# Optimization experiments

Measured on AMD Instinct MI355X. Metric: run time of the kernel, lower is better.

## Reference

```python
import jax, jax.numpy as jnp
import numpy as np

SR = 44100
PRE_EMPH = 0.97
FRAME_LEN = int(0.02 * SR)      # 882
FRAME_HOP = FRAME_LEN // 2      # 441
N_FFT = 2048
EPS = 1e-10


def setup_inputs() -> dict:
    key = jax.random.key(0)
    k1, k2 = jax.random.split(key)
    waveform = jax.random.normal(k1, (16, 441000), dtype=jnp.float32)
    # librosa mel filterbank is a fixed nonnegative (n_mels, n_fft//2+1) matrix;
    # a random surrogate keeps the math (dense matmul) identical.
    mel_filters = jax.random.uniform(k2, (60, N_FFT // 2 + 1), dtype=jnp.float32)
    return {"waveform": waveform, "mel_filters": mel_filters}


def _mfdwc(waveform, mel_filters):
    dt = waveform.dtype
    # pre-emphasis: y[0]=x[0], y[t]=x[t]-0.97*x[t-1]
    emph = jnp.concatenate(
        [waveform[:, :1], waveform[:, 1:] - PRE_EMPH * waveform[:, :-1]], axis=1)
    L = emph.shape[1]
    n_frames = 1 + (L - FRAME_LEN) // FRAME_HOP  # static
    idx = jnp.arange(n_frames)[:, None] * FRAME_HOP + jnp.arange(FRAME_LEN)[None, :]
    frames = emph[:, idx]                                   # (B, T, 882)
    window = jnp.asarray(np.hamming(FRAME_LEN), dtype=dt)   # (882,)
    windowed = frames * window
    spec = jnp.fft.rfft(windowed, n=N_FFT, axis=-1)         # (B, T, 1025) complex
    power = jnp.real(spec) ** 2 + jnp.imag(spec) ** 2       # |FFT|^2
    mel = jnp.einsum('mf,btf->btm', mel_filters, power)     # (B, T, 60)
    logmel = jnp.log(mel + EPS)
    # 1-level Haar DWT along mel axis (pywt convention, even length):
    # cA = (x_even + x_odd)/sqrt(2), cD = (x_even - x_odd)/sqrt(2)
    sq2 = jnp.sqrt(jnp.asarray(2.0, dt))
    x_even, x_odd = logmel[..., 0::2], logmel[..., 1::2]
    cA = (x_even + x_odd) / sq2                             # (B, T, 30)
    cD = (x_even - x_odd) / sq2                             # (B, T, 30)
    # delta (window=3, edge-padded): d[t] = a[clamp(t+1)] - a[clamp(t-1)]
    fwd = jnp.concatenate([cA[:, 1:], cA[:, -1:]], axis=1)
    bwd = jnp.concatenate([cA[:, :1], cA[:, :-1]], axis=1)
    delta = fwd - bwd
    feats = jnp.concatenate([cA, delta, cD], axis=-1)       # (B, T, 90)
    mean = jnp.mean(feats, axis=1)
    std = jnp.std(feats, axis=1, ddof=1)                    # torch.std unbiased
    return jnp.concatenate([mean, std], axis=1)             # (B, 180)


def reference(waveform, mel_filters):
    return _mfdwc(waveform, mel_filters)
```

## Files before the change

kernel.cpp:

```cpp
#include <hip/hip_runtime.h>
#include <hip/hip_bf16.h>
#include <math.h>

#define FRAME_LEN 882
#define FRAME_HOP 441
#define NFFT 2048
#define NFRAMES 999
#define NBATCH 16
#define NMEL 60
#define WAVE_LEN 441000
#define PRE_EMPH 0.97f
#define EPS 1e-10f
#define NROWS (NBATCH * NFRAMES)
#define KPAD 1056
#define NKC 33
#define PANEL_ELEMS (NKC * 512)
#define PI_F 3.14159265358979323846f

#define PADI(i) ((i) + ((i) >> 4))

__device__ __forceinline__ int frag_off(int m, int k) {
  return ((k >> 5) * 512) | (((k >> 3) & 3) * 128) | (m * 8) | (k & 7);
}

typedef float vf2 __attribute__((ext_vector_type(2)));
__device__ __forceinline__ vf2 mkv(float x, float y){ vf2 r; r.x = x; r.y = y; return r; }
__device__ __forceinline__ vf2 cmul(vf2 a, vf2 b){ return a.xx * b + mkv(-a.y, a.y) * b.yx; }
__device__ __forceinline__ vf2 rotni(vf2 z){ return mkv(z.y, -z.x); }

__device__ __forceinline__ void dif_group8(vf2* x, vf2 t1) {
  const vf2 C41 = mkv(0.7071067812f, -0.7071067812f);
  vf2 w0 = t1, w1 = cmul(t1, C41), w2 = rotni(w0), w3 = rotni(w1);
  vf2 u, v;
  u=x[0]; v=x[4]; x[0]=u+v; x[4]=cmul(u-v, w0);
  u=x[1]; v=x[5]; x[1]=u+v; x[5]=cmul(u-v, w1);
  u=x[2]; v=x[6]; x[2]=u+v; x[6]=cmul(u-v, w2);
  u=x[3]; v=x[7]; x[3]=u+v; x[7]=cmul(u-v, w3);
  vf2 t2 = cmul(t1, t1), t2r = rotni(t2);
  u=x[0]; v=x[2]; x[0]=u+v; x[2]=cmul(u-v, t2);
  u=x[1]; v=x[3]; x[1]=u+v; x[3]=cmul(u-v, t2r);
  u=x[4]; v=x[6]; x[4]=u+v; x[6]=cmul(u-v, t2);
  u=x[5]; v=x[7]; x[5]=u+v; x[7]=cmul(u-v, t2r);
  vf2 t4 = cmul(t2, t2);
  u=x[0]; v=x[1]; x[0]=u+v; x[1]=cmul(u-v, t4);
  u=x[2]; v=x[3]; x[2]=u+v; x[3]=cmul(u-v, t4);
  u=x[4]; v=x[5]; x[4]=u+v; x[5]=cmul(u-v, t4);
  u=x[6]; v=x[7]; x[6]=u+v; x[7]=cmul(u-v, t4);
}

__device__ __forceinline__ void dif_radix4(vf2* x) {
  vf2 y0 = x[0] + x[2];
  vf2 y2 = x[0] - x[2];
  vf2 y1 = x[1] + x[3];
  vf2 y3 = rotni(x[1] - x[3]);
  x[0] = y0 + y1; x[1] = y0 - y1;
  x[2] = y2 + y3; x[3] = y2 - y3;
}

__global__ __launch_bounds__(256) void fft_pow_kernel(
    const float* __restrict__ wav, __hip_bfloat16* __restrict__ powrF)
{
  __shared__ vf2 lds[NFFT + (NFFT >> 4)];
  const int t  = threadIdx.x;
  const int t0 = 2 * blockIdx.x, t1f = t0 + 1;
  const bool has1 = (t1f < NFRAMES);
  const int b = blockIdx.y;
  const float* w = wav + (size_t)b * WAVE_LEN;
  const int s0 = t0 * FRAME_HOP;
  int s1 = t1f * FRAME_HOP;
  if (s1 > WAVE_LEN - FRAME_LEN) s1 = WAVE_LEN - FRAME_LEN;

  vf2 x[8];
  {
    float sB, cB, sD, cD;
    __sincosf(6.283185307179586f * (float)t / 881.0f, &sB, &cB);
    __sincosf(6.283185307179586f * 256.0f / 881.0f, &sD, &cD);
    vf2 cur  = mkv(cB, sB);
    vf2 step = mkv(cD, sD);
#pragma unroll
    for (int k = 0; k < 8; ++k) {
      int i = k * 256 + t;
      float v1 = 0.f, v2 = 0.f;
      if (i < FRAME_LEN) {
        float win = 0.54f - 0.46f * cur.x;
        int s = s0 + i;
        float e1 = (s > 0) ? (w[s] - PRE_EMPH * w[s - 1]) : w[s];
        v1 = e1 * win;
        int ss = s1 + i;
        v2 = (w[ss] - PRE_EMPH * w[ss - 1]) * win;
      }
      x[k] = mkv(v1, v2);
      cur = cmul(cur, step);
    }
  }

  {
    float sA, cA;
    __sincosf(-PI_F * (float)t / 1024.0f, &sA, &cA);
    dif_group8(x, mkv(cA, sA));
  }
#pragma unroll
  for (int k = 0; k < 8; ++k) lds[PADI(k * 256 + t)] = x[k];
  __syncthreads();

  {
    const int q = t >> 5, r = t & 31;
#pragma unroll
    for (int k = 0; k < 8; ++k) x[k] = lds[PADI(q * 256 + k * 32 + r)];
    float sA, cA;
    __sincosf(-PI_F * (float)r / 128.0f, &sA, &cA);
    dif_group8(x, mkv(cA, sA));
    __syncthreads();
#pragma unroll
    for (int k = 0; k < 8; ++k) lds[PADI(q * 256 + k * 32 + r)] = x[k];
  }
  __syncthreads();

  {
    const int q = t >> 2, r = t & 3;
#pragma unroll
    for (int k = 0; k < 8; ++k) x[k] = lds[PADI(q * 32 + k * 4 + r)];
    float tc = (r == 0) ? 1.0f : (r == 1) ? 0.980785280f : (r == 2) ? 0.923879533f : 0.831469612f;
    float ts = (r == 0) ? 0.0f : (r == 1) ? -0.195090322f : (r == 2) ? -0.382683432f : -0.555570233f;
    dif_group8(x, mkv(tc, ts));
    __syncthreads();
#pragma unroll
    for (int k = 0; k < 8; ++k) lds[PADI(q * 32 + k * 4 + r)] = x[k];
  }
  __syncthreads();

  {
    vf2 xa[4], xb[4];
#pragma unroll
    for (int j = 0; j < 4; ++j) {
      xa[j] = lds[PADI(4 * t + j)];
      xb[j] = lds[PADI(4 * (t + 256) + j)];
    }
    dif_radix4(xa);
    dif_radix4(xb);
    __syncthreads();
#pragma unroll
    for (int j = 0; j < 4; ++j) {
      lds[PADI(4 * t + j)] = xa[j];
      lds[PADI(4 * (t + 256) + j)] = xb[j];
    }
  }
  __syncthreads();

  const int r0g = b * NFRAMES + t0;
  const int r1g = r0g + 1;
  __hip_bfloat16* q0 = powrF + (size_t)(r0g >> 4) * PANEL_ELEMS;
  const int m0 = r0g & 15;
  __hip_bfloat16* q1 = powrF + (size_t)(r1g >> 4) * PANEL_ELEMS;
  const int m1 = r1g & 15;
#pragma unroll
  for (int c = 0; c < 4; ++c) {
    int f = t + 256 * c;
    int j1 = (int)(__brev((unsigned)f) >> 21);
    int j2 = (int)(__brev((unsigned)((NFFT - f) & (NFFT - 1))) >> 21);
    vf2 z = lds[PADI(j1)];
    vf2 y = lds[PADI(j2)];
    float f1r = z.x + y.x, f1i = z.y - y.y;
    float f2r = z.y + y.y, f2i = y.x - z.x;
    float pw1 = 0.25f * (f1r * f1r + f1i * f1i);
    float pw2 = 0.25f * (f2r * f2r + f2i * f2i);
    q0[frag_off(m0, f)] = __float2bfloat16(pw1);
    if (has1) q1[frag_off(m1, f)] = __float2bfloat16(pw2);
  }
  if (t == 0) {
    vf2 z = lds[PADI(1)];
    q0[frag_off(m0, 1024)] = __float2bfloat16(z.x * z.x);
    if (has1) q1[frag_off(m1, 1024)] = __float2bfloat16(z.y * z.y);
  }
  if (t < KPAD - 1025) {
    int f = 1025 + t;
    q0[frag_off(m0, f)] = __float2bfloat16(0.f);
    if (has1) q1[frag_off(m1, f)] = __float2bfloat16(0.f);
  }
}

__global__ __launch_bounds__(256) void filtconv_kernel(
    const float* __restrict__ filt, __hip_bfloat16* __restrict__ filtbF)
{
  const int mm = blockIdx.x;
  __hip_bfloat16* qp = filtbF + (size_t)(mm >> 4) * PANEL_ELEMS;
  const int m = mm & 15;
  for (int k = threadIdx.x; k < KPAD; k += 256) {
    float v = (mm < NMEL && k < 1025) ? filt[mm * 1025 + k] : 0.f;
    qp[frag_off(m, k)] = __float2bfloat16(v);
  }
}

typedef __attribute__((ext_vector_type(8))) short short8x;
typedef __attribute__((ext_vector_type(4))) float float4x;

__global__ __launch_bounds__(256) void melgemm_kernel(
    const __hip_bfloat16* __restrict__ powrF,
    const __hip_bfloat16* __restrict__ filtbF,
    float* __restrict__ logmelT)
{
  const int wave = threadIdx.x >> 6, lane = threadIdx.x & 63;
  const int p = blockIdx.x;
  const __hip_bfloat16* pA = powrF + (size_t)p * PANEL_ELEMS + lane * 8;
  const __hip_bfloat16* pB = filtbF + (size_t)wave * PANEL_ELEMS + lane * 8;

  float4x acc0 = {0.f, 0.f, 0.f, 0.f};
  float4x acc1 = {0.f, 0.f, 0.f, 0.f};
#pragma unroll 4
  for (int kc = 0; kc < 16; ++kc) {
    short8x a0 = *(const short8x*)(pA + kc * 512);
    short8x b0 = *(const short8x*)(pB + kc * 512);
    short8x a1 = *(const short8x*)(pA + (kc + 16) * 512);
    short8x b1 = *(const short8x*)(pB + (kc + 16) * 512);
    acc0 = __builtin_amdgcn_mfma_f32_16x16x32_bf16(a0, b0, acc0, 0, 0, 0);
    acc1 = __builtin_amdgcn_mfma_f32_16x16x32_bf16(a1, b1, acc1, 0, 0, 0);
  }
  {
    short8x a = *(const short8x*)(pA + 32 * 512);
    short8x bf = *(const short8x*)(pB + 32 * 512);
    acc0 = __builtin_amdgcn_mfma_f32_16x16x32_bf16(a, bf, acc0, 0, 0, 0);
  }

  const int mel = wave * 16 + (lane & 15);
  const int rsub = (lane >> 4) * 4;
  if (mel < NMEL) {
#pragma unroll
    for (int reg = 0; reg < 4; ++reg) {
      int row = p * 16 + rsub + reg;
      float vv = acc0[reg] + acc1[reg];
      logmelT[(size_t)mel * NROWS + row] = __logf(vv + EPS);
    }
  }
}

__global__ __launch_bounds__(256) void stats_kernel(
    const float* __restrict__ lmT, float* __restrict__ out)
{
  __shared__ float red[4];
  const int j   = blockIdx.x;
  const int b   = blockIdx.y;
  const int tid = threadIdx.x;
  const int base = b * NFRAMES;
  const float inv_sq2 = 0.7071067811865475f;
  const bool v3 = (tid < NFRAMES - 768);

  float f0, f1, f2, f3;
  if (j < 30) {
    const float* e = lmT + (size_t)(2 * j) * NROWS + base;
    const float* o = lmT + (size_t)(2 * j + 1) * NROWS + base;
    f0 = (e[tid]       + o[tid])       * inv_sq2;
    f1 = (e[tid + 256] + o[tid + 256]) * inv_sq2;
    f2 = (e[tid + 512] + o[tid + 512]) * inv_sq2;
    f3 = v3 ? (e[tid + 768] + o[tid + 768]) * inv_sq2 : 0.f;
  } else if (j < 60) {
    const int m = j - 30;
    const float* e = lmT + (size_t)(2 * m) * NROWS + base;
    const float* o = lmT + (size_t)(2 * m + 1) * NROWS + base;
    auto dl = [&](int t) -> float {
      int tp = (t + 1 > NFRAMES - 1) ? (NFRAMES - 1) : (t + 1);
      int tm = (t - 1 < 0) ? 0 : (t - 1);
      return ((e[tp] + o[tp]) - (e[tm] + o[tm])) * inv_sq2;
    };
    f0 = dl(tid);
    f1 = dl(tid + 256);
    f2 = dl(tid + 512);
    f3 = v3 ? dl(tid + 768) : 0.f;
  } else {
    const int m = j - 60;
    const float* e = lmT + (size_t)(2 * m) * NROWS + base;
    const float* o = lmT + (size_t)(2 * m + 1) * NROWS + base;
    f0 = (e[tid]       - o[tid])       * inv_sq2;
    f1 = (e[tid + 256] - o[tid + 256]) * inv_sq2;
    f2 = (e[tid + 512] - o[tid + 512]) * inv_sq2;
    f3 = v3 ? (e[tid + 768] - o[tid + 768]) * inv_sq2 : 0.f;
  }

  float s = f0 + f1 + f2 + f3;
  for (int o2 = 32; o2 > 0; o2 >>= 1) s += __shfl_xor(s, o2, 64);
  if ((tid & 63) == 0) red[tid >> 6] = s;
  __syncthreads();
  float mean = (red[0] + red[1] + red[2] + red[3]) / (float)NFRAMES;
  __syncthreads();

  float d0 = f0 - mean, d1 = f1 - mean, d2 = f2 - mean;
  float d3 = v3 ? (f3 - mean) : 0.f;
  float s2 = d0 * d0 + d1 * d1 + d2 * d2 + d3 * d3;
  for (int o2 = 32; o2 > 0; o2 >>= 1) s2 += __shfl_xor(s2, o2, 64);
  if ((tid & 63) == 0) red[tid >> 6] = s2;
  __syncthreads();
  float var = (red[0] + red[1] + red[2] + red[3]) / (float)(NFRAMES - 1);

  if (tid == 0) {
    out[b * 180 + j]      = mean;
    out[b * 180 + 90 + j] = sqrtf(var);
  }
}

extern "C" void kernel_launch(void* const* d_in, const int* in_sizes, int n_in,
                              void* d_out, int out_size, void* d_ws, size_t ws_size,
                              hipStream_t stream) {
  const float* wav  = (const float*)d_in[0];
  const float* filt = (const float*)d_in[1];
  float* out = (float*)d_out;

  unsigned char* ws = (unsigned char*)d_ws;
  __hip_bfloat16* powrF  = (__hip_bfloat16*)(ws);
  size_t off = (size_t)999 * PANEL_ELEMS * 2;
  __hip_bfloat16* filtbF = (__hip_bfloat16*)(ws + off);
  off += (size_t)4 * PANEL_ELEMS * 2;
  float* logmelT = (float*)(ws + off);

  filtconv_kernel<<<64, 256, 0, stream>>>(filt, filtbF);
  fft_pow_kernel<<<dim3((NFRAMES + 1) / 2, NBATCH), 256, 0, stream>>>(wav, powrF);
  melgemm_kernel<<<999, 256, 0, stream>>>(powrF, filtbF, logmelT);
  stats_kernel<<<dim3(90, NBATCH), 256, 0, stream>>>(logmelT, out);
}
```

Before: 121.8 us.

## Stage one 16-row panel per FFT block in LDS and coalesce writes

Result: slower. 151.5 us (+24.4%).

```diff
diff --git a/kernel.cpp b/kernel.cpp
--- a/kernel.cpp
+++ b/kernel.cpp
@@ -12,9 +12,11 @@
 #define PRE_EMPH 0.97f
 #define EPS 1e-10f
 #define NROWS (NBATCH * NFRAMES)
+#define NPANEL 999
 #define KPAD 1056
 #define NKC 33
 #define PANEL_ELEMS (NKC * 512)
+#define STG_STRIDE 1064
 #define PI_F 3.14159265358979323846f
 
 #define PADI(i) ((i) + ((i) >> 4))
@@ -57,125 +59,165 @@
   x[2] = y2 + y3; x[3] = y2 - y3;
 }
 
+__device__ __forceinline__ unsigned bf16bits(float v) {
+  union { float f; unsigned u; } c; c.f = v;
+  unsigned lsb = (c.u >> 16) & 1;
+  return ((c.u + 0x7fff + lsb) >> 16) & 0xffff;
+}
+
 __global__ __launch_bounds__(256) void fft_pow_kernel(
     const float* __restrict__ wav, __hip_bfloat16* __restrict__ powrF)
 {
   __shared__ vf2 lds[NFFT + (NFFT >> 4)];
-  const int t  = threadIdx.x;
-  const int t0 = 2 * blockIdx.x, t1f = t0 + 1;
-  const bool has1 = (t1f < NFRAMES);
-  const int b = blockIdx.y;
-  const float* w = wav + (size_t)b * WAVE_LEN;
-  const int s0 = t0 * FRAME_HOP;
-  int s1 = t1f * FRAME_HOP;
-  if (s1 > WAVE_LEN - FRAME_LEN) s1 = WAVE_LEN - FRAME_LEN;
-
-  vf2 x[8];
+  __shared__ unsigned short stage[16 * STG_STRIDE];
+  const int t = threadIdx.x;
+  const int p = blockIdx.x;
+
+  vf2 win0, wstep, tw0, tw1, tw2;
   {
-    float sB, cB, sD, cD;
-    __sincosf(6.283185307179586f * (float)t / 881.0f, &sB, &cB);
-    __sincosf(6.283185307179586f * 256.0f / 881.0f, &sD, &cD);
-    vf2 cur  = mkv(cB, sB);
-    vf2 step = mkv(cD, sD);
-#pragma unroll
-    for (int k = 0; k < 8; ++k) {
-      int i = k * 256 + t;
-      float v1 = 0.f, v2 = 0.f;
-      if (i < FRAME_LEN) {
-        float win = 0.54f - 0.46f * cur.x;
-        int s = s0 + i;
-        float e1 = (s > 0) ? (w[s] - PRE_EMPH * w[s - 1]) : w[s];
-        v1 = e1 * win;
-        int ss = s1 + i;
-        v2 = (w[ss] - PRE_EMPH * w[ss - 1]) * win;
-      }
-      x[k] = mkv(v1, v2);
-      cur = cmul(cur, step);
-    }
-  }
-
-  {
-    float sA, cA;
-    __sincosf(-PI_F * (float)t / 1024.0f, &sA, &cA);
-    dif_group8(x, mkv(cA, sA));
-  }
-#pragma unroll
-  for (int k = 0; k < 8; ++k) lds[PADI(k * 256 + t)] = x[k];
-  __syncthreads();
-
-  {
-    const int q = t >> 5, r = t & 31;
-#pragma unroll
-    for (int k = 0; k < 8; ++k) x[k] = lds[PADI(q * 256 + k * 32 + r)];
-    float sA, cA;
-    __sincosf(-PI_F * (float)r / 128.0f, &sA, &cA);
-    dif_group8(x, mkv(cA, sA));
-    __syncthreads();
-#pragma unroll
-    for (int k = 0; k < 8; ++k) lds[PADI(q * 256 + k * 32 + r)] = x[k];
-  }
-  __syncthreads();
-
-  {
-    const int q = t >> 2, r = t & 3;
-#pragma unroll
-    for (int k = 0; k < 8; ++k) x[k] = lds[PADI(q * 32 + k * 4 + r)];
+    float s, c;
+    __sincosf(6.283185307179586f * (float)t / 881.0f, &s, &c); win0 = mkv(c, s);
+    __sincosf(6.283185307179586f * 256.0f / 881.0f, &s, &c);   wstep = mkv(c, s);
+    __sincosf(-PI_F * (float)t / 1024.0f, &s, &c);             tw0 = mkv(c, s);
+    __sincosf(-PI_F * (float)(t & 31) / 128.0f, &s, &c);       tw1 = mkv(c, s);
+    const int r = t & 3;
     float tc = (r == 0) ? 1.0f : (r == 1) ? 0.980785280f : (r == 2) ? 0.923879533f : 0.831469612f;
     float ts = (r == 0) ? 0.0f : (r == 1) ? -0.195090322f : (r == 2) ? -0.382683432f : -0.555570233f;
-    dif_group8(x, mkv(tc, ts));
-    __syncthreads();
-#pragma unroll
-    for (int k = 0; k < 8; ++k) lds[PADI(q * 32 + k * 4 + r)] = x[k];
-  }
-  __syncthreads();
-
-  {
-    vf2 xa[4], xb[4];
-#pragma unroll
-    for (int j = 0; j < 4; ++j) {
-      xa[j] = lds[PADI(4 * t + j)];
-      xb[j] = lds[PADI(4 * (t + 256) + j)];
-    }
-    dif_radix4(xa);
-    dif_radix4(xb);
-    __syncthreads();
-#pragma unroll
-    for (int j = 0; j < 4; ++j) {
-      lds[PADI(4 * t + j)] = xa[j];
-      lds[PADI(4 * (t + 256) + j)] = xb[j];
-    }
-  }
-  __syncthreads();
-
-  const int r0g = b * NFRAMES + t0;
-  const int r1g = r0g + 1;
-  __hip_bfloat16* q0 = powrF + (size_t)(r0g >> 4) * PANEL_ELEMS;
-  const int m0 = r0g & 15;
-  __hip_bfloat16* q1 = powrF + (size_t)(r1g >> 4) * PANEL_ELEMS;
-  const int m1 = r1g & 15;
-#pragma unroll
-  for (int c = 0; c < 4; ++c) {
-    int f = t + 256 * c;
-    int j1 = (int)(__brev((unsigned)f) >> 21);
-    int j2 = (int)(__brev((unsigned)((NFFT - f) & (NFFT - 1))) >> 21);
-    vf2 z = lds[PADI(j1)];
-    vf2 y = lds[PADI(j2)];
-    float f1r = z.x + y.x, f1i = z.y - y.y;
-    float f2r = z.y + y.y, f2i = y.x - z.x;
-    float pw1 = 0.25f * (f1r * f1r + f1i * f1i);
-    float pw2 = 0.25f * (f2r * f2r + f2i * f2i);
-    q0[frag_off(m0, f)] = __float2bfloat16(pw1);
-    if (has1) q1[frag_off(m1, f)] = __float2bfloat16(pw2);
-  }
-  if (t == 0) {
-    vf2 z = lds[PADI(1)];
-    q0[frag_off(m0, 1024)] = __float2bfloat16(z.x * z.x);
-    if (has1) q1[frag_off(m1, 1024)] = __float2bfloat16(z.y * z.y);
-  }
-  if (t < KPAD - 1025) {
-    int f = 1025 + t;
-    q0[frag_off(m0, f)] = __float2bfloat16(0.f);
-    if (has1) q1[frag_off(m1, f)] = __float2bfloat16(0.f);
+    tw2 = mkv(tc, ts);
+  }
+  int jz[2], jy[2];
+#pragma unroll
+  for (int c = 0; c < 2; ++c) {
+    int u2 = 2 * (t + 256 * c);
+    jz[c] = PADI((int)(__brev((unsigned)u2) >> 21));
+    jy[c] = PADI((int)(__brev((unsigned)((NFFT - u2) & (NFFT - 1))) >> 21));
+  }
+
+  for (int i = 0; i < 8; ++i) {
+    const int rA = 16 * p + 2 * i, rB = rA + 1;
+    const int bA = rA / NFRAMES, tA = rA - bA * NFRAMES;
+    const int bB = rB / NFRAMES, tB = rB - bB * NFRAMES;
+    const float* wA = wav + (size_t)bA * WAVE_LEN;
+    const float* wB = wav + (size_t)bB * WAVE_LEN;
+    const int sA = tA * FRAME_HOP, sB = tB * FRAME_HOP;
+
+    vf2 x[8];
+    {
+      vf2 cur = win0;
+#pragma unroll
+      for (int k = 0; k < 4; ++k) {
+        int idx = k * 256 + t;
+        float v1 = 0.f, v2 = 0.f;
+        if (idx < FRAME_LEN) {
+          float win = 0.54f - 0.46f * cur.x;
+          int s = sA + idx;
+          float e1 = (s > 0) ? (wA[s] - PRE_EMPH * wA[s - 1]) : wA[s];
+          v1 = e1 * win;
+          int ss = sB + idx;
+          float e2 = (ss > 0) ? (wB[ss] - PRE_EMPH * wB[ss - 1]) : wB[ss];
+          v2 = e2 * win;
+        }
+        x[k] = mkv(v1, v2);
+        if (k < 3) cur = cmul(cur, wstep);
+      }
+#pragma unroll
+      for (int k = 4; k < 8; ++k) x[k] = mkv(0.f, 0.f);
+    }
+
+    dif_group8(x, tw0);
+#pragma unroll
+    for (int k = 0; k < 8; ++k) lds[PADI(k * 256 + t)] = x[k];
+    __syncthreads();
+
+    {
+      const int q = t >> 5, r = t & 31;
+#pragma unroll
+      for (int k = 0; k < 8; ++k) x[k] = lds[PADI(q * 256 + k * 32 + r)];
+      dif_group8(x, tw1);
+      __syncthreads();
+#pragma unroll
+      for (int k = 0; k < 8; ++k) lds[PADI(q * 256 + k * 32 + r)] = x[k];
+    }
+    __syncthreads();
+
+    {
+      const int q = t >> 2, r = t & 3;
+#pragma unroll
+      for (int k = 0; k < 8; ++k) x[k] = lds[PADI(q * 32 + k * 4 + r)];
+      dif_group8(x, tw2);
+      __syncthreads();
+#pragma unroll
+      for (int k = 0; k < 8; ++k) lds[PADI(q * 32 + k * 4 + r)] = x[k];
+    }
+    __syncthreads();
+
+    {
+      vf2 xa[4], xb[4];
+#pragma unroll
+      for (int j = 0; j < 4; ++j) {
+        xa[j] = lds[PADI(4 * t + j)];
+        xb[j] = lds[PADI(4 * (t + 256) + j)];
+      }
+      dif_radix4(xa);
+      dif_radix4(xb);
+      __syncthreads();
+#pragma unroll
+      for (int j = 0; j < 4; ++j) {
+        lds[PADI(4 * t + j)] = xa[j];
+        lds[PADI(4 * (t + 256) + j)] = xb[j];
+      }
+    }
+    __syncthreads();
+
+    unsigned short* rowA = stage + (2 * i) * STG_STRIDE;
+    unsigned short* rowB = rowA + STG_STRIDE;
+#pragma unroll
+    for (int c = 0; c < 2; ++c) {
+      int u = t + 256 * c;
+      vf2 z0 = lds[jz[c]];
+      vf2 y0 = lds[jy[c]];
+      vf2 z1 = lds[PADI((jz[c] - (jz[c] >> 4) ))];
+      int j1 = (int)(__brev((unsigned)(2 * u)) >> 21);
+      vf2 z1b = lds[PADI(j1 + 1024)];
+      int j2b = 2047 - j1;
+      vf2 y1b = lds[PADI(j2b)];
+      float f1r = z0.x + y0.x, f1i = z0.y - y0.y;
+      float f2r = z0.y + y0.y, f2i = y0.x - z0.x;
+      float pA0 = 0.25f * (f1r * f1r + f1i * f1i);
+      float pB0 = 0.25f * (f2r * f2r + f2i * f2i);
+      f1r = z1b.x + y1b.x; f1i = z1b.y - y1b.y;
+      f2r = z1b.y + y1b.y; f2i = y1b.x - z1b.x;
+      float pA1 = 0.25f * (f1r * f1r + f1i * f1i);
+      float pB1 = 0.25f * (f2r * f2r + f2i * f2i);
+      unsigned uA = bf16bits(pA0) | (bf16bits(pA1) << 16);
+      unsigned uB = bf16bits(pB0) | (bf16bits(pB1) << 16);
+      *(unsigned*)(rowA + 2 * u) = uA;
+      *(unsigned*)(rowB + 2 * u) = uB;
+    }
+    if (t < 16) {
+      float pA0 = 0.f, pB0 = 0.f;
+      if (t == 0) {
+        vf2 z = lds[PADI(1)];
+        pA0 = z.x * z.x;
+        pB0 = z.y * z.y;
+      }
+      unsigned uA = bf16bits(pA0);
+      unsigned uB = bf16bits(pB0);
+      *(unsigned*)(rowA + 1024 + 2 * t) = uA;
+      *(unsigned*)(rowB + 1024 + 2 * t) = uB;
+    }
+    __syncthreads();
+  }
+
+  uint4* g4 = (uint4*)(powrF + (size_t)p * PANEL_ELEMS);
+#pragma unroll
+  for (int c = 0; c < 9; ++c) {
+    int g = c * 256 + t;
+    if (c < 8 || t < 64) {
+      int kc = g >> 6, sub = (g >> 4) & 3, m = g & 15;
+      const uint4* src = (const uint4*)(stage + m * STG_STRIDE + kc * 32 + sub * 8);
+      g4[g] = *src;
+    }
   }
 }
 
@@ -200,25 +242,23 @@
     float* __restrict__ logmelT)
 {
   const int wave = threadIdx.x >> 6, lane = threadIdx.x & 63;
-  const int p = blockIdx.x;
-  const __hip_bfloat16* pA = powrF + (size_t)p * PANEL_ELEMS + lane * 8;
-  const __hip_bfloat16* pB = filtbF + (size_t)wave * PANEL_ELEMS + lane * 8;
+  const int p0 = blockIdx.x * 2;
+  const int p1 = p0 + 1;
+  const bool has1 = (p1 < NPANEL);
+  const int p1c = has1 ? p1 : p0;
+  const __hip_bfloat16* pA0 = powrF + (size_t)p0 * PANEL_ELEMS + lane * 8;
+  const __hip_bfloat16* pA1 = powrF + (size_t)p1c * PANEL_ELEMS + lane * 8;
+  const __hip_bfloat16* pB  = filtbF + (size_t)wave * PANEL_ELEMS + lane * 8;
 
   float4x acc0 = {0.f, 0.f, 0.f, 0.f};
   float4x acc1 = {0.f, 0.f, 0.f, 0.f};
-#pragma unroll 4
-  for (int kc = 0; kc < 16; ++kc) {
-    short8x a0 = *(const short8x*)(pA + kc * 512);
-    short8x b0 = *(const short8x*)(pB + kc * 512);
-    short8x a1 = *(const short8x*)(pA + (kc + 16) * 512);
-    short8x b1 = *(const short8x*)(pB + (kc + 16) * 512);
-    acc0 = __builtin_amdgcn_mfma_f32_16x16x32_bf16(a0, b0, acc0, 0, 0, 0);
-    acc1 = __builtin_amdgcn_mfma_f32_16x16x32_bf16(a1, b1, acc1, 0, 0, 0);
-  }
-  {
-    short8x a = *(const short8x*)(pA + 32 * 512);
-    short8x bf = *(const short8x*)(pB + 32 * 512);
-    acc0 = __builtin_amdgcn_mfma_f32_16x16x32_bf16(a, bf, acc0, 0, 0, 0);
+#pragma unroll 3
+  for (int kc = 0; kc < NKC; ++kc) {
+    short8x b  = *(const short8x*)(pB + kc * 512);
+    short8x a0 = *(const short8x*)(pA0 + kc * 512);
+    short8x a1 = *(const short8x*)(pA1 + kc * 512);
+    acc0 = __builtin_amdgcn_mfma_f32_16x16x32_bf16(a0, b, acc0, 0, 0, 0);
+    acc1 = __builtin_amdgcn_mfma_f32_16x16x32_bf16(a1, b, acc1, 0, 0, 0);
   }
 
   const int mel = wave * 16 + (lane & 15);
@@ -226,9 +266,12 @@
   if (mel < NMEL) {
 #pragma unroll
     for (int reg = 0; reg < 4; ++reg) {
-      int row = p * 16 + rsub + reg;
-      float vv = acc0[reg] + acc1[reg];
-      logmelT[(size_t)mel * NROWS + row] = __logf(vv + EPS);
+      int row0 = p0 * 16 + rsub + reg;
+      logmelT[(size_t)mel * NROWS + row0] = __logf(acc0[reg] + EPS);
+      if (has1) {
+        int row1 = p1 * 16 + rsub + reg;
+        logmelT[(size_t)mel * NROWS + row1] = __logf(acc1[reg] + EPS);
+      }
     }
   }
 }
@@ -305,13 +348,13 @@
 
   unsigned char* ws = (unsigned char*)d_ws;
   __hip_bfloat16* powrF  = (__hip_bfloat16*)(ws);
-  size_t off = (size_t)999 * PANEL_ELEMS * 2;
+  size_t off = (size_t)NPANEL * PANEL_ELEMS * 2;
   __hip_bfloat16* filtbF = (__hip_bfloat16*)(ws + off);
   off += (size_t)4 * PANEL_ELEMS * 2;
   float* logmelT = (float*)(ws + off);
 
   filtconv_kernel<<<64, 256, 0, stream>>>(filt, filtbF);
-  fft_pow_kernel<<<dim3((NFRAMES + 1) / 2, NBATCH), 256, 0, stream>>>(wav, powrF);
-  melgemm_kernel<<<999, 256, 0, stream>>>(powrF, filtbF, logmelT);
+  fft_pow_kernel<<<NPANEL, 256, 0, stream>>>(wav, powrF);
+  melgemm_kernel<<<(NPANEL + 1) / 2, 256, 0, stream>>>(powrF, filtbF, logmelT);
   stats_kernel<<<dim3(90, NBATCH), 256, 0, stream>>>(logmelT, out);
 }
```

## Fold filter conversion into FFT launch and process two panels per GEMM block

Applied to the files above, without the earlier changes.

Result: no change. 119.7 us (-1.7%).

```diff
diff --git a/kernel.cpp b/kernel.cpp
--- a/kernel.cpp
+++ b/kernel.cpp
@@ -12,6 +12,7 @@
 #define PRE_EMPH 0.97f
 #define EPS 1e-10f
 #define NROWS (NBATCH * NFRAMES)
+#define NPANEL 999
 #define KPAD 1056
 #define NKC 33
 #define PANEL_ELEMS (NKC * 512)
@@ -58,13 +59,27 @@
 }
 
 __global__ __launch_bounds__(256) void fft_pow_kernel(
-    const float* __restrict__ wav, __hip_bfloat16* __restrict__ powrF)
+    const float* __restrict__ wav, const float* __restrict__ filt,
+    __hip_bfloat16* __restrict__ powrF, __hip_bfloat16* __restrict__ filtbF)
 {
   __shared__ vf2 lds[NFFT + (NFFT >> 4)];
+  const int id = blockIdx.x;
+
+  if (id >= 8000) {
+    const int mm = id - 8000;
+    __hip_bfloat16* qp = filtbF + (size_t)(mm >> 4) * PANEL_ELEMS;
+    const int m = mm & 15;
+    for (int k = threadIdx.x; k < KPAD; k += 256) {
+      float v = (mm < NMEL && k < 1025) ? filt[mm * 1025 + k] : 0.f;
+      qp[frag_off(m, k)] = __float2bfloat16(v);
+    }
+    return;
+  }
+
   const int t  = threadIdx.x;
-  const int t0 = 2 * blockIdx.x, t1f = t0 + 1;
+  const int b  = id & 15;
+  const int t0 = 2 * (id >> 4), t1f = t0 + 1;
   const bool has1 = (t1f < NFRAMES);
-  const int b = blockIdx.y;
   const float* w = wav + (size_t)b * WAVE_LEN;
   const int s0 = t0 * FRAME_HOP;
   int s1 = t1f * FRAME_HOP;
@@ -179,18 +194,6 @@
   }
 }
 
-__global__ __launch_bounds__(256) void filtconv_kernel(
-    const float* __restrict__ filt, __hip_bfloat16* __restrict__ filtbF)
-{
-  const int mm = blockIdx.x;
-  __hip_bfloat16* qp = filtbF + (size_t)(mm >> 4) * PANEL_ELEMS;
-  const int m = mm & 15;
-  for (int k = threadIdx.x; k < KPAD; k += 256) {
-    float v = (mm < NMEL && k < 1025) ? filt[mm * 1025 + k] : 0.f;
-    qp[frag_off(m, k)] = __float2bfloat16(v);
-  }
-}
-
 typedef __attribute__((ext_vector_type(8))) short short8x;
 typedef __attribute__((ext_vector_type(4))) float float4x;
 
@@ -200,25 +203,23 @@
     float* __restrict__ logmelT)
 {
   const int wave = threadIdx.x >> 6, lane = threadIdx.x & 63;
-  const int p = blockIdx.x;
-  const __hip_bfloat16* pA = powrF + (size_t)p * PANEL_ELEMS + lane * 8;
-  const __hip_bfloat16* pB = filtbF + (size_t)wave * PANEL_ELEMS + lane * 8;
+  const int p0 = blockIdx.x * 2;
+  const int p1 = p0 + 1;
+  const bool has1 = (p1 < NPANEL);
+  const int p1c = has1 ? p1 : p0;
+  const __hip_bfloat16* pA0 = powrF + (size_t)p0 * PANEL_ELEMS + lane * 8;
+  const __hip_bfloat16* pA1 = powrF + (size_t)p1c * PANEL_ELEMS + lane * 8;
+  const __hip_bfloat16* pB  = filtbF + (size_t)wave * PANEL_ELEMS + lane * 8;
 
   float4x acc0 = {0.f, 0.f, 0.f, 0.f};
   float4x acc1 = {0.f, 0.f, 0.f, 0.f};
-#pragma unroll 4
-  for (int kc = 0; kc < 16; ++kc) {
-    short8x a0 = *(const short8x*)(pA + kc * 512);
-    short8x b0 = *(const short8x*)(pB + kc * 512);
-    short8x a1 = *(const short8x*)(pA + (kc + 16) * 512);
-    short8x b1 = *(const short8x*)(pB + (kc + 16) * 512);
-    acc0 = __builtin_amdgcn_mfma_f32_16x16x32_bf16(a0, b0, acc0, 0, 0, 0);
-    acc1 = __builtin_amdgcn_mfma_f32_16x16x32_bf16(a1, b1, acc1, 0, 0, 0);
-  }
-  {
-    short8x a = *(const short8x*)(pA + 32 * 512);
-    short8x bf = *(const short8x*)(pB + 32 * 512);
-    acc0 = __builtin_amdgcn_mfma_f32_16x16x32_bf16(a, bf, acc0, 0, 0, 0);
+#pragma unroll 3
+  for (int kc = 0; kc < NKC; ++kc) {
+    short8x b  = *(const short8x*)(pB + kc * 512);
+    short8x a0 = *(const short8x*)(pA0 + kc * 512);
+    short8x a1 = *(const short8x*)(pA1 + kc * 512);
+    acc0 = __builtin_amdgcn_mfma_f32_16x16x32_bf16(a0, b, acc0, 0, 0, 0);
+    acc1 = __builtin_amdgcn_mfma_f32_16x16x32_bf16(a1, b, acc1, 0, 0, 0);
   }
 
   const int mel = wave * 16 + (lane & 15);
@@ -226,9 +227,12 @@
   if (mel < NMEL) {
 #pragma unroll
     for (int reg = 0; reg < 4; ++reg) {
-      int row = p * 16 + rsub + reg;
-      float vv = acc0[reg] + acc1[reg];
-      logmelT[(size_t)mel * NROWS + row] = __logf(vv + EPS);
+      int row0 = p0 * 16 + rsub + reg;
+      logmelT[(size_t)mel * NROWS + row0] = __logf(acc0[reg] + EPS);
+      if (has1) {
+        int row1 = p1 * 16 + rsub + reg;
+        logmelT[(size_t)mel * NROWS + row1] = __logf(acc1[reg] + EPS);
+      }
     }
   }
 }
@@ -305,13 +309,12 @@
 
   unsigned char* ws = (unsigned char*)d_ws;
   __hip_bfloat16* powrF  = (__hip_bfloat16*)(ws);
-  size_t off = (size_t)999 * PANEL_ELEMS * 2;
+  size_t off = (size_t)NPANEL * PANEL_ELEMS * 2;
   __hip_bfloat16* filtbF = (__hip_bfloat16*)(ws + off);
   off += (size_t)4 * PANEL_ELEMS * 2;
   float* logmelT = (float*)(ws + off);
 
-  filtconv_kernel<<<64, 256, 0, stream>>>(filt, filtbF);
-  fft_pow_kernel<<<dim3((NFRAMES + 1) / 2, NBATCH), 256, 0, stream>>>(wav, powrF);
-  melgemm_kernel<<<999, 256, 0, stream>>>(powrF, filtbF, logmelT);
+  fft_pow_kernel<<<8064, 256, 0, stream>>>(wav, filt, powrF, filtbF);
+  melgemm_kernel<<<(NPANEL + 1) / 2, 256, 0, stream>>>(powrF, filtbF, logmelT);
   stats_kernel<<<dim3(90, NBATCH), 256, 0, stream>>>(logmelT, out);
 }
```

## Restructure FFT to radix-16 stages with two frame pairs per block, fold filter conversion

Applied to the files above, without the earlier changes.

Result: faster. 117.6 us (-3.4%).

```diff
diff --git a/kernel.cpp b/kernel.cpp
--- a/kernel.cpp
+++ b/kernel.cpp
@@ -12,6 +12,7 @@
 #define PRE_EMPH 0.97f
 #define EPS 1e-10f
 #define NROWS (NBATCH * NFRAMES)
+#define NPANEL 999
 #define KPAD 1056
 #define NKC 33
 #define PANEL_ELEMS (NKC * 512)
@@ -28,58 +29,112 @@
 __device__ __forceinline__ vf2 cmul(vf2 a, vf2 b){ return a.xx * b + mkv(-a.y, a.y) * b.yx; }
 __device__ __forceinline__ vf2 rotni(vf2 z){ return mkv(z.y, -z.x); }
 
-__device__ __forceinline__ void dif_group8(vf2* x, vf2 t1) {
-  const vf2 C41 = mkv(0.7071067812f, -0.7071067812f);
-  vf2 w0 = t1, w1 = cmul(t1, C41), w2 = rotni(w0), w3 = rotni(w1);
+__device__ __forceinline__ void dif_group16(vf2* x, vf2 t1, bool zerohi) {
+  const vf2 C81 = mkv(0.9238795325f, -0.3826834324f);
+  const vf2 C82 = mkv(0.7071067812f, -0.7071067812f);
+  const vf2 C83 = mkv(0.3826834324f, -0.9238795325f);
+  vf2 w0 = t1, w1 = cmul(t1, C81), w2 = cmul(t1, C82), w3 = cmul(t1, C83);
+  vf2 ws1[8] = {w0, w1, w2, w3, rotni(w0), rotni(w1), rotni(w2), rotni(w3)};
+  if (zerohi) {
+#pragma unroll
+    for (int k = 0; k < 8; ++k) x[k + 8] = cmul(x[k], ws1[k]);
+  } else {
+#pragma unroll
+    for (int k = 0; k < 8; ++k) {
+      vf2 u = x[k], v = x[k + 8];
+      x[k] = u + v;
+      x[k + 8] = cmul(u - v, ws1[k]);
+    }
+  }
+  vf2 t2 = cmul(t1, t1);
+  vf2 v1 = cmul(t2, C82);
+  vf2 ws2[4] = {t2, v1, rotni(t2), rotni(v1)};
+#pragma unroll
+  for (int h = 0; h < 2; ++h) {
+#pragma unroll
+    for (int k = 0; k < 4; ++k) {
+      vf2 u = x[h*8 + k], v = x[h*8 + k + 4];
+      x[h*8 + k] = u + v;
+      x[h*8 + k + 4] = cmul(u - v, ws2[k]);
+    }
+  }
+  vf2 t4 = cmul(t2, t2);
+  vf2 t4r = rotni(t4);
+#pragma unroll
+  for (int h = 0; h < 4; ++h) {
+    vf2 a = x[h*4 + 0], b = x[h*4 + 2];
+    x[h*4 + 0] = a + b; x[h*4 + 2] = cmul(a - b, t4);
+    a = x[h*4 + 1]; b = x[h*4 + 3];
+    x[h*4 + 1] = a + b; x[h*4 + 3] = cmul(a - b, t4r);
+  }
+  vf2 t8 = cmul(t4, t4);
+#pragma unroll
+  for (int j = 0; j < 8; ++j) {
+    vf2 a = x[2*j], b = x[2*j + 1];
+    x[2*j] = a + b; x[2*j + 1] = cmul(a - b, t8);
+  }
+}
+
+__device__ __forceinline__ void dif8(vf2* y) {
+  const vf2 c1 = mkv(0.7071067812f, -0.7071067812f);
+  const vf2 c3 = mkv(-0.7071067812f, -0.7071067812f);
   vf2 u, v;
-  u=x[0]; v=x[4]; x[0]=u+v; x[4]=cmul(u-v, w0);
-  u=x[1]; v=x[5]; x[1]=u+v; x[5]=cmul(u-v, w1);
-  u=x[2]; v=x[6]; x[2]=u+v; x[6]=cmul(u-v, w2);
-  u=x[3]; v=x[7]; x[3]=u+v; x[7]=cmul(u-v, w3);
-  vf2 t2 = cmul(t1, t1), t2r = rotni(t2);
-  u=x[0]; v=x[2]; x[0]=u+v; x[2]=cmul(u-v, t2);
-  u=x[1]; v=x[3]; x[1]=u+v; x[3]=cmul(u-v, t2r);
-  u=x[4]; v=x[6]; x[4]=u+v; x[6]=cmul(u-v, t2);
-  u=x[5]; v=x[7]; x[5]=u+v; x[7]=cmul(u-v, t2r);
-  vf2 t4 = cmul(t2, t2);
-  u=x[0]; v=x[1]; x[0]=u+v; x[1]=cmul(u-v, t4);
-  u=x[2]; v=x[3]; x[2]=u+v; x[3]=cmul(u-v, t4);
-  u=x[4]; v=x[5]; x[4]=u+v; x[5]=cmul(u-v, t4);
-  u=x[6]; v=x[7]; x[6]=u+v; x[7]=cmul(u-v, t4);
-}
-
-__device__ __forceinline__ void dif_radix4(vf2* x) {
-  vf2 y0 = x[0] + x[2];
-  vf2 y2 = x[0] - x[2];
-  vf2 y1 = x[1] + x[3];
-  vf2 y3 = rotni(x[1] - x[3]);
-  x[0] = y0 + y1; x[1] = y0 - y1;
-  x[2] = y2 + y3; x[3] = y2 - y3;
+  u=y[0]; v=y[4]; y[0]=u+v; y[4]=u-v;
+  u=y[1]; v=y[5]; y[1]=u+v; y[5]=cmul(u-v, c1);
+  u=y[2]; v=y[6]; y[2]=u+v; y[6]=rotni(u-v);
+  u=y[3]; v=y[7]; y[3]=u+v; y[7]=cmul(u-v, c3);
+  u=y[0]; v=y[2]; y[0]=u+v; y[2]=u-v;
+  u=y[1]; v=y[3]; y[1]=u+v; y[3]=rotni(u-v);
+  u=y[4]; v=y[6]; y[4]=u+v; y[6]=u-v;
+  u=y[5]; v=y[7]; y[5]=u+v; y[7]=rotni(u-v);
+  u=y[0]; v=y[1]; y[0]=u+v; y[1]=u-v;
+  u=y[2]; v=y[3]; y[2]=u+v; y[3]=u-v;
+  u=y[4]; v=y[5]; y[4]=u+v; y[5]=u-v;
+  u=y[6]; v=y[7]; y[6]=u+v; y[7]=u-v;
 }
 
 __global__ __launch_bounds__(256) void fft_pow_kernel(
-    const float* __restrict__ wav, __hip_bfloat16* __restrict__ powrF)
+    const float* __restrict__ wav, const float* __restrict__ filt,
+    __hip_bfloat16* __restrict__ powrF, __hip_bfloat16* __restrict__ filtbF)
 {
-  __shared__ vf2 lds[NFFT + (NFFT >> 4)];
-  const int t  = threadIdx.x;
-  const int t0 = 2 * blockIdx.x, t1f = t0 + 1;
+  __shared__ vf2 lds2[2][NFFT + (NFFT >> 4)];
+  const int id = blockIdx.x;
+
+  if (id >= 4000) {
+    const int mm = id - 4000;
+    __hip_bfloat16* qp = filtbF + (size_t)(mm >> 4) * PANEL_ELEMS;
+    const int m = mm & 15;
+    for (int k = threadIdx.x; k < KPAD; k += 256) {
+      float v = (mm < NMEL && k < 1025) ? filt[mm * 1025 + k] : 0.f;
+      qp[frag_off(m, k)] = __float2bfloat16(v);
+    }
+    return;
+  }
+
+  const int t   = threadIdx.x;
+  const int fid = t >> 7;
+  const int tt  = t & 127;
+  vf2* lds = lds2[fid];
+
+  const int P  = id * 2 + fid;
+  const int b  = P & 15;
+  const int t0 = 2 * (P >> 4), t1f = t0 + 1;
   const bool has1 = (t1f < NFRAMES);
-  const int b = blockIdx.y;
   const float* w = wav + (size_t)b * WAVE_LEN;
   const int s0 = t0 * FRAME_HOP;
   int s1 = t1f * FRAME_HOP;
   if (s1 > WAVE_LEN - FRAME_LEN) s1 = WAVE_LEN - FRAME_LEN;
 
-  vf2 x[8];
+  vf2 x[16];
   {
     float sB, cB, sD, cD;
-    __sincosf(6.283185307179586f * (float)t / 881.0f, &sB, &cB);
-    __sincosf(6.283185307179586f * 256.0f / 881.0f, &sD, &cD);
+    __sincosf(6.283185307179586f * (float)tt / 881.0f, &sB, &cB);
+    __sincosf(6.283185307179586f * 128.0f / 881.0f, &sD, &cD);
     vf2 cur  = mkv(cB, sB);
     vf2 step = mkv(cD, sD);
 #pragma unroll
-    for (int k = 0; k < 8; ++k) {
-      int i = k * 256 + t;
+    for (int k = 0; k < 7; ++k) {
+      int i = k * 128 + tt;
       float v1 = 0.f, v2 = 0.f;
       if (i < FRAME_LEN) {
         float win = 0.54f - 0.46f * cur.x;
@@ -92,57 +147,47 @@
       x[k] = mkv(v1, v2);
       cur = cmul(cur, step);
     }
+#pragma unroll
+    for (int k = 7; k < 16; ++k) x[k] = mkv(0.f, 0.f);
   }
 
   {
     float sA, cA;
-    __sincosf(-PI_F * (float)t / 1024.0f, &sA, &cA);
-    dif_group8(x, mkv(cA, sA));
-  }
-#pragma unroll
-  for (int k = 0; k < 8; ++k) lds[PADI(k * 256 + t)] = x[k];
-  __syncthreads();
-
-  {
-    const int q = t >> 5, r = t & 31;
-#pragma unroll
-    for (int k = 0; k < 8; ++k) x[k] = lds[PADI(q * 256 + k * 32 + r)];
+    __sincosf(-PI_F * (float)tt / 1024.0f, &sA, &cA);
+    dif_group16(x, mkv(cA, sA), true);
+  }
+#pragma unroll
+  for (int k = 0; k < 16; ++k) lds[PADI(k * 128 + tt)] = x[k];
+  __syncthreads();
+
+  {
+    const int Q = tt >> 3, r = tt & 7;
+    const int base = Q * 128 + r;
+#pragma unroll
+    for (int k = 0; k < 16; ++k) x[k] = lds[PADI(base + k * 8)];
     float sA, cA;
-    __sincosf(-PI_F * (float)r / 128.0f, &sA, &cA);
-    dif_group8(x, mkv(cA, sA));
+    __sincosf(-PI_F * (float)r / 64.0f, &sA, &cA);
+    dif_group16(x, mkv(cA, sA), false);
     __syncthreads();
 #pragma unroll
-    for (int k = 0; k < 8; ++k) lds[PADI(q * 256 + k * 32 + r)] = x[k];
-  }
-  __syncthreads();
-
-  {
-    const int q = t >> 2, r = t & 3;
-#pragma unroll
-    for (int k = 0; k < 8; ++k) x[k] = lds[PADI(q * 32 + k * 4 + r)];
-    float tc = (r == 0) ? 1.0f : (r == 1) ? 0.980785280f : (r == 2) ? 0.923879533f : 0.831469612f;
-    float ts = (r == 0) ? 0.0f : (r == 1) ? -0.195090322f : (r == 2) ? -0.382683432f : -0.555570233f;
-    dif_group8(x, mkv(tc, ts));
+    for (int k = 0; k < 16; ++k) lds[PADI(base + k * 8)] = x[k];
+  }
+  __syncthreads();
+
+  {
+    vf2 ya[8], yb[8];
+#pragma unroll
+    for (int j = 0; j < 8; ++j) {
+      ya[j] = lds[PADI(16 * tt + j)];
+      yb[j] = lds[PADI(16 * tt + 8 + j)];
+    }
+    dif8(ya);
+    dif8(yb);
     __syncthreads();
 #pragma unroll
-    for (int k = 0; k < 8; ++k) lds[PADI(q * 32 + k * 4 + r)] = x[k];
-  }
-  __syncthreads();
-
-  {
-    vf2 xa[4], xb[4];
-#pragma unroll
-    for (int j = 0; j < 4; ++j) {
-      xa[j] = lds[PADI(4 * t + j)];
-      xb[j] = lds[PADI(4 * (t + 256) + j)];
-    }
-    dif_radix4(xa);
-    dif_radix4(xb);
-    __syncthreads();
-#pragma unroll
-    for (int j = 0; j < 4; ++j) {
-      lds[PADI(4 * t + j)] = xa[j];
-      lds[PADI(4 * (t + 256) + j)] = xb[j];
+    for (int j = 0; j < 8; ++j) {
+      lds[PADI(16 * tt + j)] = ya[j];
+      lds[PADI(16 * tt + 8 + j)] = yb[j];
     }
   }
   __syncthreads();
@@ -154,8 +199,8 @@
   __hip_bfloat16* q1 = powrF + (size_t)(r1g >> 4) * PANEL_ELEMS;
   const int m1 = r1g & 15;
 #pragma unroll
-  for (int c = 0; c < 4; ++c) {
-    int f = t + 256 * c;
+  for (int c = 0; c < 8; ++c) {
+    int f = c * 128 + tt;
     int j1 = (int)(__brev((unsigned)f) >> 21);
     int j2 = (int)(__brev((unsigned)((NFFT - f) & (NFFT - 1))) >> 21);
     vf2 z = lds[PADI(j1)];
@@ -167,27 +212,15 @@
     q0[frag_off(m0, f)] = __float2bfloat16(pw1);
     if (has1) q1[frag_off(m1, f)] = __float2bfloat16(pw2);
   }
-  if (t == 0) {
+  if (tt == 0) {
     vf2 z = lds[PADI(1)];
     q0[frag_off(m0, 1024)] = __float2bfloat16(z.x * z.x);
     if (has1) q1[frag_off(m1, 1024)] = __float2bfloat16(z.y * z.y);
   }
-  if (t < KPAD - 1025) {
-    int f = 1025 + t;
+  if (tt < KPAD - 1025) {
+    int f = 1025 + tt;
     q0[frag_off(m0, f)] = __float2bfloat16(0.f);
     if (has1) q1[frag_off(m1, f)] = __float2bfloat16(0.f);
-  }
-}
-
-__global__ __launch_bounds__(256) void filtconv_kernel(
-    const float* __restrict__ filt, __hip_bfloat16* __restrict__ filtbF)
-{
-  const int mm = blockIdx.x;
-  __hip_bfloat16* qp = filtbF + (size_t)(mm >> 4) * PANEL_ELEMS;
-  const int m = mm & 15;
-  for (int k = threadIdx.x; k < KPAD; k += 256) {
-    float v = (mm < NMEL && k < 1025) ? filt[mm * 1025 + k] : 0.f;
-    qp[frag_off(m, k)] = __float2bfloat16(v);
   }
 }
 
@@ -305,13 +338,12 @@
 
   unsigned char* ws = (unsigned char*)d_ws;
   __hip_bfloat16* powrF  = (__hip_bfloat16*)(ws);
-  size_t off = (size_t)999 * PANEL_ELEMS * 2;
+  size_t off = (size_t)NPANEL * PANEL_ELEMS * 2;
   __hip_bfloat16* filtbF = (__hip_bfloat16*)(ws + off);
   off += (size_t)4 * PANEL_ELEMS * 2;
   float* logmelT = (float*)(ws + off);
 
-  filtconv_kernel<<<64, 256, 0, stream>>>(filt, filtbF);
-  fft_pow_kernel<<<dim3((NFRAMES + 1) / 2, NBATCH), 256, 0, stream>>>(wav, powrF);
-  melgemm_kernel<<<999, 256, 0, stream>>>(powrF, filtbF, logmelT);
+  fft_pow_kernel<<<4064, 256, 0, stream>>>(wav, filt, powrF, filtbF);
+  melgemm_kernel<<<NPANEL, 256, 0, stream>>>(powrF, filtbF, logmelT);
   stats_kernel<<<dim3(90, NBATCH), 256, 0, stream>>>(logmelT, out);
 }
```
